# Optimization experiments

Hardware: AMD Instinct MI355X
Metric: run time of the kernel (lower is better)

Reference implementation:

```python
import jax, jax.numpy as jnp
import numpy as np
from jax import lax

B, C_IN, HC, H, W, K = 32, 32, 64, 64, 64, 3


def _conv(x, w, b):
    # x: [B,C,H,W], w: [O,I,K,K] -> [B,O,H,W] (stride 1, pad 1)
    y = lax.conv_general_dilated(x, w, window_strides=(1, 1), padding=[(1, 1), (1, 1)],
                                 dimension_numbers=("NCHW", "OIHW", "NCHW"))
    return y + b[None, :, None, None]


def setup_inputs() -> dict:
    key = jax.random.key(0)
    ks = jax.random.split(key, 20)
    d = {
        "x": jax.random.normal(ks[0], (B, C_IN, H, W), jnp.float32),
        "hidden_state": jax.random.normal(ks[1], (B, HC, H, W), jnp.float32),
        "cell_state": jax.random.normal(ks[2], (B, HC, H, W), jnp.float32),
    }
    sx = 1.0 / np.sqrt(C_IN * K * K)
    sh = 1.0 / np.sqrt(HC * K * K)
    names_x = ["w_xi", "w_xf", "w_xo", "w_xg"]
    names_h = ["w_hi", "w_hf", "w_ho", "w_hg"]
    for i, n in enumerate(names_x):
        d[n] = jax.random.uniform(ks[3 + i], (HC, C_IN, K, K), jnp.float32, -sx, sx)
        d["b" + n[1:]] = jax.random.uniform(ks[7 + i], (HC,), jnp.float32, -sx, sx)
    for i, n in enumerate(names_h):
        d[n] = jax.random.uniform(ks[11 + i], (HC, HC, K, K), jnp.float32, -sh, sh)
        d["b" + n[1:]] = jax.random.uniform(ks[15 + i], (HC,), jnp.float32, -sh, sh)
    return d


def reference(x, hidden_state, cell_state,
              w_xi, w_xf, w_xo, w_xg, b_xi, b_xf, b_xo, b_xg,
              w_hi, w_hf, w_ho, w_hg, b_hi, b_hf, b_ho, b_hg):
    Wx = jnp.concatenate([w_xi, w_xf, w_xo, w_xg], axis=0)
    bx = jnp.concatenate([b_xi, b_xf, b_xo, b_xg], axis=0)
    Wh = jnp.concatenate([w_hi, w_hf, w_ho, w_hg], axis=0)
    bh = jnp.concatenate([b_hi, b_hf, b_ho, b_hg], axis=0)
    gates = _conv(x, Wx, bx) + _conv(hidden_state, Wh, bh)  # [B,4*HC,H,W]
    zi, zf, zo, zg = jnp.split(gates, 4, axis=1)
    i = jax.nn.sigmoid(zi)
    f = jax.nn.sigmoid(zf)
    o = jax.nn.sigmoid(zo)
    g = jnp.tanh(zg)
    c_new = f * cell_state + i * g
    h_new = o * jnp.tanh(c_new)
    return (h_new, c_new)
```

## Files before the change

### kernel.cpp

```cpp
#include <hip/hip_runtime.h>


#define B_   32
#define CIN  32
#define HC_  64
#define HH   64
#define WW   64

#define A_ELEMS (9 * 8 * 6 * 64 * 8)
#define P_ROW   (12 * 66 * 8)
#define SLAB    24576

typedef __attribute__((ext_vector_type(8)))  short  short8;
typedef __attribute__((ext_vector_type(16))) float  floatx16;

struct PackArgs {
    const float* wx[4]; const float* wh[4];
    const float* bx[4]; const float* bh[4];
};

__device__ __forceinline__ short f2bf(float f) {
    unsigned u = __float_as_uint(f);
    u += 0x7FFFu + ((u >> 16) & 1u);
    return (short)(u >> 16);
}

__device__ __forceinline__ void gl_lds16(const short* g, short* l) {
    __builtin_amdgcn_global_load_lds(
        (const __attribute__((address_space(1))) unsigned int*)g,
        (__attribute__((address_space(3))) unsigned int*)l, 16, 0, 0);
}

__global__ __launch_bounds__(256) void pack_weights(PackArgs pa, short* a_pk, float* bias) {
    int idx = blockIdx.x * 256 + threadIdx.x;
    if (idx < A_ELEMS) {
        int j    = idx & 7;
        int lane = (idx >> 3) & 63;
        int rest = idx >> 9;
        int kk   = rest % 6;
        int rest2 = rest / 6;
        int s    = rest2 % 8;
        int tap  = rest2 / 8;
        int og = s >> 1, fi = s & 1;
        int m32 = lane & 31;
        int gate = 2 * fi + (m32 >> 4);
        int oc   = og * 16 + (m32 & 15);
        int c    = kk * 16 + (lane >> 5) * 8 + j;
        int ky = tap / 3, kx = tap - 3 * ky;
        float v = (c < CIN)
            ? pa.wx[gate][((oc * CIN + c) * 3 + ky) * 3 + kx]
            : pa.wh[gate][((oc * HC_ + (c - CIN)) * 3 + ky) * 3 + kx];
        a_pk[idx] = f2bf(v);
    }
    if (idx < 256) {
        int gate = idx >> 6, oc = idx & 63;
        bias[idx] = pa.bx[gate][oc] + pa.bh[gate][oc];
    }
}

__global__ __launch_bounds__(256) void pack_input(const float* __restrict__ x,
                                                  const float* __restrict__ h,
                                                  short* __restrict__ P) {
    const int yy = blockIdx.x, b = blockIdx.y;
    int4* prow4 = (int4*)(P + ((size_t)b * 66 + yy) * P_ROW);

    if (yy == 0 || yy == 65) {
        int4 z = {0, 0, 0, 0};
        for (int g = threadIdx.x; g < 792; g += 256) prow4[g] = z;
        return;
    }

    __shared__ short t[64 * 98];
    const int y = yy - 1;
    const int col = threadIdx.x & 63, cg = threadIdx.x >> 6;
    for (int c = cg; c < 96; c += 4) {
        float v = (c < CIN) ? x[((b * CIN + c) * HH + y) * WW + col]
                            : h[((b * HC_ + (c - CIN)) * HH + y) * WW + col];
        t[col * 98 + c] = f2bf(v);
    }
    __syncthreads();

    for (int g = threadIdx.x; g < 792; g += 256) {
        int pc = g / 66, xx = g - 66 * pc;
        int4 val = {0, 0, 0, 0};
        if (xx >= 1 && xx <= 64) {
            const short* sp = &t[(xx - 1) * 98 + pc * 8];
            val.x = *(const int*)(sp + 0); val.y = *(const int*)(sp + 2);
            val.z = *(const int*)(sp + 4); val.w = *(const int*)(sp + 6);
        }
        prow4[g] = val;
    }
}

__global__ __launch_bounds__(512, 4) void convlstm_main(
    const short* __restrict__ P, const short* __restrict__ a_pk,
    const float* __restrict__ bias, const float* __restrict__ cell,
    float* __restrict__ out)
{
    __shared__ __align__(16) short As[SLAB];

    const int tid = threadIdx.x;
    const int b  = blockIdx.x >> 5;
    const int y0 = (blockIdx.x & 31) * 2;

    const int wv = tid >> 6, lane = tid & 63;
    const int ln31 = lane & 31, hg = lane >> 5;
    const int og = wv & 3, nh = wv >> 2;
    const int y = y0 + nh;

    floatx16 acc[2][2];
    #pragma unroll
    for (int fi = 0; fi < 2; ++fi)
        #pragma unroll
        for (int ns = 0; ns < 2; ++ns)
            #pragma unroll
            for (int q = 0; q < 16; ++q) acc[fi][ns][q] = 0.f;

    const int a_base = og * 12 * 64 * 8 + lane * 8;
    const int lnoff  = (hg * 66 + ln31) * 8;

    for (int ky = 0; ky < 3; ++ky)
    for (int kx = 0; kx < 3; ++kx) {
        const int tap = ky * 3 + kx;
        {
            const short* slab = a_pk + tap * SLAB;
            #pragma unroll
            for (int i = 0; i < 6; ++i) {
                int id = i * 512 + tid;
                gl_lds16(slab + id * 8, As + (i * 512 + wv * 64) * 8);
            }
        }
        __syncthreads();

        const short* Brow = P + ((size_t)(b * 66) + y + ky) * P_ROW + kx * 8 + lnoff;

        #pragma unroll
        for (int kk = 0; kk < 6; ++kk) {
            short8 a0 = *(const short8*)&As[a_base + (0 * 6 + kk) * 512];
            short8 a1 = *(const short8*)&As[a_base + (1 * 6 + kk) * 512];
            short8 b0 = *(const short8*)&Brow[(2 * kk * 66 + 0 ) * 8];
            short8 b1 = *(const short8*)&Brow[(2 * kk * 66 + 32) * 8];
            acc[0][0] = __builtin_amdgcn_mfma_f32_32x32x16_bf16(a0, b0, acc[0][0], 0, 0, 0);
            acc[0][1] = __builtin_amdgcn_mfma_f32_32x32x16_bf16(a0, b1, acc[0][1], 0, 0, 0);
            acc[1][0] = __builtin_amdgcn_mfma_f32_32x32x16_bf16(a1, b0, acc[1][0], 0, 0, 0);
            acc[1][1] = __builtin_amdgcn_mfma_f32_32x32x16_bf16(a1, b1, acc[1][1], 0, 0, 0);
        }
        __syncthreads();
    }

    const size_t plane = (size_t)B_ * HC_ * HH * WW;
    #pragma unroll
    for (int q = 0; q < 4; ++q)
    #pragma unroll
    for (int b8 = 0; b8 < 2; ++b8) {
        const int oc16 = q + 4 * hg + 8 * b8;
        const int oc = og * 16 + oc16;
        const float Bi = bias[oc],       Bf = bias[64 + oc];
        const float Bo = bias[128 + oc], Bg = bias[192 + oc];
        const int r_lo = q + 4 * b8, r_hi = q + 4 * (2 + b8);
        #pragma unroll
        for (int ns = 0; ns < 2; ++ns) {
            float zi = acc[0][ns][r_lo] + Bi;
            float zf = acc[0][ns][r_hi] + Bf;
            float zo = acc[1][ns][r_lo] + Bo;
            float zg = acc[1][ns][r_hi] + Bg;
            float ig = 1.f / (1.f + __expf(-zi));
            float fg = 1.f / (1.f + __expf(-zf));
            float sg = 1.f / (1.f + __expf(-zo));
            float e2 = __expf(2.f * zg);
            float gg = 1.f - 2.f / (e2 + 1.f);
            const int x = ns * 32 + ln31;
            size_t off = ((size_t)(b * HC_ + oc) * HH + y) * WW + x;
            float cn = fg * cell[off] + ig * gg;
            float ec = __expf(2.f * cn);
            out[off] = sg * (1.f - 2.f / (ec + 1.f));
            out[plane + off] = cn;
        }
    }
}

extern "C" void kernel_launch(void* const* d_in, const int* in_sizes, int n_in,
                              void* d_out, int out_size, void* d_ws, size_t ws_size,
                              hipStream_t stream) {
    PackArgs pa;
    pa.wx[0] = (const float*)d_in[3];  pa.bx[0] = (const float*)d_in[4];
    pa.wx[1] = (const float*)d_in[5];  pa.bx[1] = (const float*)d_in[6];
    pa.wx[2] = (const float*)d_in[7];  pa.bx[2] = (const float*)d_in[8];
    pa.wx[3] = (const float*)d_in[9];  pa.bx[3] = (const float*)d_in[10];
    pa.wh[0] = (const float*)d_in[11]; pa.bh[0] = (const float*)d_in[12];
    pa.wh[1] = (const float*)d_in[13]; pa.bh[1] = (const float*)d_in[14];
    pa.wh[2] = (const float*)d_in[15]; pa.bh[2] = (const float*)d_in[16];
    pa.wh[3] = (const float*)d_in[17]; pa.bh[3] = (const float*)d_in[18];

    short* a_pk = (short*)d_ws;
    float* bias = (float*)((char*)d_ws + A_ELEMS * sizeof(short));
    short* P    = (short*)((char*)d_ws + 443392);

    pack_weights<<<dim3(A_ELEMS / 256), dim3(256), 0, stream>>>(pa, a_pk, bias);
    pack_input <<<dim3(66, B_), dim3(256), 0, stream>>>(
        (const float*)d_in[0], (const float*)d_in[1], P);
    convlstm_main<<<dim3(B_ * 32), dim3(512), 0, stream>>>(
        P, a_pk, bias, (const float*)d_in[2], (float*)d_out);
}
```

Before: 227.9 us.

## Make weights LDS-resident per output group and double-buffer B-fragment loads

Reorganizes the main kernel so each block handles one output-channel group across 8 rows. All 9 taps of that group's packed weights are loaded into LDS once at the start, which removes the per-tap global-to-LDS load and its two barriers. The input-fragment loads are restructured so the three kx taps share one row pointer, and the next kk step's fragments are prefetched while the current one computes. In exchange, LDS use per block rises (about 110 KB), occupancy is capped at 2 blocks per CU, and each row of input is read by 4 blocks instead of 1.

```diff
diff --git a/kernel.cpp b/kernel.cpp
--- a/kernel.cpp
+++ b/kernel.cpp
@@ -7,9 +7,9 @@
 #define HH   64
 #define WW   64
 
-#define A_ELEMS (9 * 8 * 6 * 64 * 8)
+#define OG_SLAB (9 * 2 * 6 * 64 * 8)
+#define A_ELEMS (4 * OG_SLAB)
 #define P_ROW   (12 * 66 * 8)
-#define SLAB    24576
 
 typedef __attribute__((ext_vector_type(8)))  short  short8;
 typedef __attribute__((ext_vector_type(16))) float  floatx16;
@@ -38,10 +38,11 @@
         int lane = (idx >> 3) & 63;
         int rest = idx >> 9;
         int kk   = rest % 6;
-        int rest2 = rest / 6;
-        int s    = rest2 % 8;
-        int tap  = rest2 / 8;
-        int og = s >> 1, fi = s & 1;
+        int r2   = rest / 6;
+        int fi   = r2 & 1;
+        int r3   = r2 >> 1;
+        int tap  = r3 % 9;
+        int og   = r3 / 9;
         int m32 = lane & 31;
         int gate = 2 * fi + (m32 >> 4);
         int oc   = og * 16 + (m32 & 15);
@@ -92,21 +93,32 @@
     }
 }
 
-__global__ __launch_bounds__(512, 4) void convlstm_main(
+__global__ __launch_bounds__(512, 2) void convlstm_main(
     const short* __restrict__ P, const short* __restrict__ a_pk,
     const float* __restrict__ bias, const float* __restrict__ cell,
     float* __restrict__ out)
 {
-    __shared__ __align__(16) short As[SLAB];
+    __shared__ __align__(16) short As[OG_SLAB];
 
     const int tid = threadIdx.x;
-    const int b  = blockIdx.x >> 5;
-    const int y0 = (blockIdx.x & 31) * 2;
+    const int og = blockIdx.x >> 8;
+    const int b  = (blockIdx.x >> 3) & 31;
+    const int rg = blockIdx.x & 7;
 
     const int wv = tid >> 6, lane = tid & 63;
     const int ln31 = lane & 31, hg = lane >> 5;
-    const int og = wv & 3, nh = wv >> 2;
-    const int y = y0 + nh;
+    const int y = rg * 8 + wv;
+
+    {
+        const short* src = a_pk + og * OG_SLAB;
+        #pragma unroll
+        for (int i = 0; i < 14; ++i) {
+            int id = i * 512 + tid;
+            if (id < 6912)
+                gl_lds16(src + id * 8, As + (i * 512 + wv * 64) * 8);
+        }
+    }
+    __syncthreads();
 
     floatx16 acc[2][2];
     #pragma unroll
@@ -116,36 +128,40 @@
             #pragma unroll
             for (int q = 0; q < 16; ++q) acc[fi][ns][q] = 0.f;
 
-    const int a_base = og * 12 * 64 * 8 + lane * 8;
+    const int albase = lane * 8;
     const int lnoff  = (hg * 66 + ln31) * 8;
 
-    for (int ky = 0; ky < 3; ++ky)
-    for (int kx = 0; kx < 3; ++kx) {
-        const int tap = ky * 3 + kx;
-        {
-            const short* slab = a_pk + tap * SLAB;
+    for (int ky = 0; ky < 3; ++ky) {
+        const short* Brow = P + ((size_t)(b * 66) + y + ky) * P_ROW + lnoff;
+        short8 bf[2][3][2];
+        #pragma unroll
+        for (int kx = 0; kx < 3; ++kx)
             #pragma unroll
-            for (int i = 0; i < 6; ++i) {
-                int id = i * 512 + tid;
-                gl_lds16(slab + id * 8, As + (i * 512 + wv * 64) * 8);
+            for (int ns = 0; ns < 2; ++ns)
+                bf[0][kx][ns] = *(const short8*)&Brow[kx * 8 + ns * 256];
+
+        #pragma unroll
+        for (int kk = 0; kk < 6; ++kk) {
+            const int cur = kk & 1, nxt = cur ^ 1;
+            if (kk < 5) {
+                #pragma unroll
+                for (int kx = 0; kx < 3; ++kx)
+                    #pragma unroll
+                    for (int ns = 0; ns < 2; ++ns)
+                        bf[nxt][kx][ns] =
+                            *(const short8*)&Brow[(kk + 1) * 1056 + kx * 8 + ns * 256];
             }
-        }
-        __syncthreads();
-
-        const short* Brow = P + ((size_t)(b * 66) + y + ky) * P_ROW + kx * 8 + lnoff;
-
-        #pragma unroll
-        for (int kk = 0; kk < 6; ++kk) {
-            short8 a0 = *(const short8*)&As[a_base + (0 * 6 + kk) * 512];
-            short8 a1 = *(const short8*)&As[a_base + (1 * 6 + kk) * 512];
-            short8 b0 = *(const short8*)&Brow[(2 * kk * 66 + 0 ) * 8];
-            short8 b1 = *(const short8*)&Brow[(2 * kk * 66 + 32) * 8];
-            acc[0][0] = __builtin_amdgcn_mfma_f32_32x32x16_bf16(a0, b0, acc[0][0], 0, 0, 0);
-            acc[0][1] = __builtin_amdgcn_mfma_f32_32x32x16_bf16(a0, b1, acc[0][1], 0, 0, 0);
-            acc[1][0] = __builtin_amdgcn_mfma_f32_32x32x16_bf16(a1, b0, acc[1][0], 0, 0, 0);
-            acc[1][1] = __builtin_amdgcn_mfma_f32_32x32x16_bf16(a1, b1, acc[1][1], 0, 0, 0);
-        }
-        __syncthreads();
+            #pragma unroll
+            for (int kx = 0; kx < 3; ++kx) {
+                const int tap = ky * 3 + kx;
+                short8 a0 = *(const short8*)&As[((tap * 2 + 0) * 6 + kk) * 512 + albase];
+                short8 a1 = *(const short8*)&As[((tap * 2 + 1) * 6 + kk) * 512 + albase];
+                acc[0][0] = __builtin_amdgcn_mfma_f32_32x32x16_bf16(a0, bf[cur][kx][0], acc[0][0], 0, 0, 0);
+                acc[0][1] = __builtin_amdgcn_mfma_f32_32x32x16_bf16(a0, bf[cur][kx][1], acc[0][1], 0, 0, 0);
+                acc[1][0] = __builtin_amdgcn_mfma_f32_32x32x16_bf16(a1, bf[cur][kx][0], acc[1][0], 0, 0, 0);
+                acc[1][1] = __builtin_amdgcn_mfma_f32_32x32x16_bf16(a1, bf[cur][kx][1], acc[1][1], 0, 0, 0);
+            }
+        }
     }
 
     const size_t plane = (size_t)B_ * HC_ * HH * WW;
@@ -199,6 +215,6 @@
     pack_weights<<<dim3(A_ELEMS / 256), dim3(256), 0, stream>>>(pa, a_pk, bias);
     pack_input <<<dim3(66, B_), dim3(256), 0, stream>>>(
         (const float*)d_in[0], (const float*)d_in[1], P);
-    convlstm_main<<<dim3(B_ * 32), dim3(512), 0, stream>>>(
+    convlstm_main<<<dim3(1024), dim3(512), 0, stream>>>(
         P, a_pk, bias, (const float*)d_in[2], (float*)d_out);
 }
```

New measurement: 234.1 us. 1.03x slower.
